# Kernel optimization log

Hardware: AMD Instinct MI355X
Metric: run time of the kernel (lower is better)

## Reference

```python
import jax, jax.numpy as jnp
import numpy as np

H = 4          # num_heads
MB = 4         # ttt mini_batch_size
GRP = 4        # scan_checkpoint_group_size
TTT_LR = 0.1   # ttt_base_lr
ERF_C = 0.7071067811865476   # 1/sqrt(2)
PDF_C = 0.3989422804014327   # 1/sqrt(2*pi)


def _gelu(z):
    return 0.5 * z * (1.0 + jax.scipy.special.erf(z * ERF_C))


def _gelu_grad(z):
    return 0.5 * (1.0 + jax.scipy.special.erf(z * ERF_C)) + z * jnp.exp(-0.5 * z * z) * PDF_C


def _ln(x, w, b, eps):
    mu = x.mean(-1, keepdims=True)
    var = ((x - mu) ** 2).mean(-1, keepdims=True)
    return w * (x - mu) / jnp.sqrt(var + eps) + b


def _ln_l2_bwd(z, w, b, target, eps=1e-6):
    # grad of 0.5*||LN(z; w, b) - target||^2 w.r.t. z (fused LN backward)
    mu = z.mean(-1, keepdims=True)
    var = ((z - mu) ** 2).mean(-1, keepdims=True)
    std = jnp.sqrt(var + eps)
    zhat = (z - mu) / std
    y = w * zhat + b
    g = w * (y - target)
    return (g - g.mean(-1, keepdims=True) - zhat * (g * zhat).mean(-1, keepdims=True)) / std


def _conv1d(x, w, b, pad):
    # x: [B, Cin, L], w: [Cout, Cin, K]
    y = jax.lax.conv_general_dilated(x, w, (1,), [(pad, pad)], dimension_numbers=("NCH", "OIH", "NCH"))
    return y + b[None, :, None]


def _ttt(x, wq, wk, wv, wo, W1, b1, W2, b2, lnw, lnb):
    # x: [B, L, D];  ttt_mlp fast-weight scan over mini-batches of size MB
    B, L, D = x.shape
    d = D // H
    nmb = L // MB
    ng = nmb // GRP

    def split(w):
        # [B,L,D] -> [ng, GRP, B, H, MB, d]
        return (x @ w).reshape(B, L, H, d).transpose(0, 2, 1, 3).reshape(B, H, ng, GRP, MB, d).transpose(2, 3, 0, 1, 4, 5)

    XQ, XK, XV = split(wq), split(wk), split(wv)
    lw = lnw[None, :, None, :]  # [1,H,1,d]
    lb = lnb[None, :, None, :]
    eta = TTT_LR / MB

    carry = (jnp.broadcast_to(W1, (B, H, d, 4 * d)),
             jnp.broadcast_to(b1, (B, H, 1, 4 * d)),
             jnp.broadcast_to(W2, (B, H, 4 * d, d)),
             jnp.broadcast_to(b2, (B, H, 1, d)))

    def step(c, inp):
        W1c, b1c, W2c, b2c = c
        xq, xk, xv = inp  # each [B,H,MB,d]
        Z1 = jnp.einsum('bhmd,bhdk->bhmk', xk, W1c) + b1c
        X2 = _gelu(Z1)
        Z2 = jnp.einsum('bhmk,bhkd->bhmd', X2, W2c) + b2c
        gZ2 = _ln_l2_bwd(Z2, lw, lb, xv - xk)
        gZ1 = jnp.einsum('bhmd,bhkd->bhmk', gZ2, W2c) * _gelu_grad(Z1)
        W1n = W1c - eta * jnp.einsum('bhmd,bhmk->bhdk', xk, gZ1)
        b1n = b1c - eta * gZ1.sum(2, keepdims=True)
        W2n = W2c - eta * jnp.einsum('bhmk,bhmd->bhkd', X2, gZ2)
        b2n = b2c - eta * gZ2.sum(2, keepdims=True)
        Z1q = jnp.einsum('bhmd,bhdk->bhmk', xq, W1n) + b1n
        Z2q = jnp.einsum('bhmk,bhkd->bhmd', _gelu(Z1q), W2n) + b2n
        return (W1n, b1n, W2n, b2n), xq + _ln(Z2q, lw, lb, 1e-6)

    @jax.checkpoint
    def group(c, inp_g):
        return jax.lax.scan(step, c, inp_g)

    _, out = jax.lax.scan(group, carry, (XQ, XK, XV))  # [ng,GRP,B,H,MB,d]
    out = out.transpose(2, 3, 0, 1, 4, 5).reshape(B, H, L, d).transpose(0, 2, 1, 3).reshape(B, L, D)
    return x + out @ wo


def reference(x, conv1_w, conv1_b, convs_w, convs_b, ln_w, ln_b, wq, wk, wv, wo,
              ttt_W1, ttt_b1, ttt_W2, ttt_b2, ttt_ln_w, ttt_ln_b,
              fc_w, fc_b, fc2_w, fc2_b, fc3_w, fc3_b):
    h = x.transpose(0, 2, 1)                       # [B, dim1, L]
    h = jax.nn.relu(_conv1d(h, conv1_w, conv1_b, 0))
    acts = []
    for i in range(8):
        h = jax.nn.relu(_conv1d(h, convs_w[i], convs_b[i], 1))
        acts.append(h)
    h = acts[1] + acts[3] + acts[5] + acts[7]      # x2 + x4 + x6 + x8
    h = h.transpose(0, 2, 1)                       # [B, L, dim3]
    h = _ln(h, ln_w, ln_b, 1e-5)
    h = _ttt(h, wq, wk, wv, wo, ttt_W1, ttt_b1, ttt_W2, ttt_b2, ttt_ln_w, ttt_ln_b)
    h = _ln(h, ln_w, ln_b, 1e-5)                   # module reuses self.layer_norm
    h = h @ fc_w + fc_b
    h = h @ fc2_w + fc2_b
    return h @ fc3_w + fc3_b                       # [B, L, 1]


def setup_inputs() -> dict:
    key = jax.random.key(0)
    ks = jax.random.split(key, 12)
    B, L, dim1, dim2, dim3 = 4, 1024, 64, 512, 256
    Hn, dh = 4, 64

    def n(k, shape):
        return jax.random.normal(k, shape, jnp.float32) * 0.02

    return {
        "x": jax.random.normal(ks[0], (B, L, dim1), jnp.float32),
        "conv1_w": n(ks[1], (dim3, dim1, 1)),
        "conv1_b": jnp.zeros((dim3,), jnp.float32),
        "convs_w": n(ks[2], (8, dim3, dim3, 3)),
        "convs_b": jnp.zeros((8, dim3), jnp.float32),
        "ln_w": jnp.ones((dim3,), jnp.float32),
        "ln_b": jnp.zeros((dim3,), jnp.float32),
        "wq": n(ks[3], (dim3, dim3)),
        "wk": n(ks[4], (dim3, dim3)),
        "wv": n(ks[5], (dim3, dim3)),
        "wo": n(ks[6], (dim3, dim3)),
        "ttt_W1": n(ks[7], (Hn, dh, 4 * dh)),
        "ttt_b1": jnp.zeros((Hn, 1, 4 * dh), jnp.float32),
        "ttt_W2": n(ks[8], (Hn, 4 * dh, dh)),
        "ttt_b2": jnp.zeros((Hn, 1, dh), jnp.float32),
        "ttt_ln_w": jnp.ones((Hn, dh), jnp.float32),
        "ttt_ln_b": jnp.zeros((Hn, dh), jnp.float32),
        "fc_w": n(ks[9], (dim3, dim2)),
        "fc_b": jnp.zeros((dim2,), jnp.float32),
        "fc2_w": n(ks[10], (dim2, dim1)),
        "fc2_b": jnp.zeros((dim1,), jnp.float32),
        "fc3_w": n(ks[11], (dim1, 1)),
        "fc3_b": jnp.zeros((1,), jnp.float32),
    }
```

## Files before the change

kernel.cpp:

```cpp
#include <hip/hip_runtime.h>
#include <hip/hip_bf16.h>


#define ERF_CF 0.70710678118654752f
#define PDF_CF 0.3989422804014327f
#define ETA 0.025f

typedef __attribute__((ext_vector_type(8))) short bfrag;
typedef __attribute__((ext_vector_type(4))) float f32x4;

union FB { bfrag v; unsigned short u[8]; unsigned d[4]; };

__device__ __forceinline__ float wsum(float v) {
#pragma unroll
  for (int o = 32; o > 0; o >>= 1) v += __shfl_xor(v, o, 64);
  return v;
}

__device__ __forceinline__ unsigned pack_split(float x) {
  unsigned u = __float_as_uint(x);
  unsigned hb = u & 0xFFFF0000u;
  float lf = x - __uint_as_float(hb);
  return hb | (__float_as_uint(lf) >> 16);
}
__device__ __forceinline__ float uns(unsigned short hs, unsigned short ls) {
  return __uint_as_float((unsigned)hs << 16) + __uint_as_float((unsigned)ls << 16);
}
__device__ __forceinline__ float fb_el(const FB& H, const FB& L, int e) {
  return __uint_as_float((unsigned)H.u[e] << 16) +
         __uint_as_float((unsigned)L.u[e] << 16);
}
__device__ __forceinline__ void split2(float f, unsigned short& hs, unsigned short& ls) {
  unsigned u = __float_as_uint(f);
  unsigned hb = u & 0xFFFF0000u;
  hs = (unsigned short)(u >> 16);
  ls = (unsigned short)(__float_as_uint(f - __uint_as_float(hb)) >> 16);
}
__device__ __forceinline__ f32x4 mm3(bfrag ah, bfrag al, bfrag bh, bfrag bl, f32x4 acc) {
  acc = __builtin_amdgcn_mfma_f32_16x16x32_bf16(ah, bh, acc, 0, 0, 0);
  acc = __builtin_amdgcn_mfma_f32_16x16x32_bf16(ah, bl, acc, 0, 0, 0);
  acc = __builtin_amdgcn_mfma_f32_16x16x32_bf16(al, bh, acc, 0, 0, 0);
  return acc;
}

__global__ void prep_w(const float* __restrict__ c1w, const float* __restrict__ cw,
                       float* __restrict__ wt1, float* __restrict__ wt) {
  int id = blockIdx.x * 256 + threadIdx.x;
  if (id < 16384) {
    int ci = id >> 8, co = id & 255;
    wt1[id] = c1w[co * 64 + ci];
  }
  int id2 = id - 16384;
  if (id2 >= 0 && id2 < 1572864) {
    int cv = id2 / 196608;
    int r = id2 - cv * 196608;
    int k = r >> 8, co = r & 255;
    int tt = k >> 8, ci = k & 255;
    wt[id2] = cw[((cv * 256 + co) * 256 + ci) * 3 + tt];
  }
}

__global__ void zero_halo(float* __restrict__ bufA, float* __restrict__ bufB) {
  int id = blockIdx.x * 256 + threadIdx.x;
  int c = id & 255;
  int row = (id >> 8) & 1;
  int b = (id >> 9) & 3;
  float* p = (id >> 11) ? bufB : bufA;
  p[(b * 1026 + row * 1025) * 256 + c] = 0.0f;
}

template <int BIAS, int RELU, int RES, int OST, int ACC>
__global__ __launch_bounds__(256) void gemm_k(
    const float* __restrict__ A, const float* __restrict__ Wt,
    const float* __restrict__ bias, const float* __restrict__ res,
    float* __restrict__ out, float* __restrict__ accp,
    int M, int N, int K, int lda, int haloA) {
  __shared__ float As[16][68];
  __shared__ float Bs[16][64];
  const int tid = threadIdx.x;
  const int bm = blockIdx.x * 64, bn = blockIdx.y * 64;
  const int tx = tid & 15, ty = tid >> 4;
  float acc[4][4] = {};

  for (int k0 = 0; k0 < K; k0 += 16) {
#pragma unroll
    for (int i = 0; i < 4; ++i) {
      int idx = tid + i * 256;
      int kk = idx & 15, mm = idx >> 4;
      int m = bm + mm;
      int rb = m * lda + (haloA ? ((m >> 10) << 9) : 0);
      As[kk][mm] = A[rb + k0 + kk];
    }
#pragma unroll
    for (int i = 0; i < 4; ++i) {
      int idx = tid + i * 256;
      int nn = idx & 63, kk = idx >> 6;
      Bs[kk][nn] = Wt[(k0 + kk) * N + bn + nn];
    }
    __syncthreads();
#pragma unroll
    for (int kk = 0; kk < 16; ++kk) {
      float4 av = *(const float4*)&As[kk][ty * 4];
      float4 bv = *(const float4*)&Bs[kk][tx * 4];
      float aa[4] = {av.x, av.y, av.z, av.w};
      float bb[4] = {bv.x, bv.y, bv.z, bv.w};
#pragma unroll
      for (int i = 0; i < 4; ++i)
#pragma unroll
        for (int j = 0; j < 4; ++j) acc[i][j] = fmaf(aa[i], bb[j], acc[i][j]);
    }
    __syncthreads();
  }

  const int n0 = bn + tx * 4;
#pragma unroll
  for (int i = 0; i < 4; ++i) {
    int m = bm + ty * 4 + i;
    int b_ = m >> 10, l = m & 1023;
    float v[4];
#pragma unroll
    for (int j = 0; j < 4; ++j) {
      float x = acc[i][j];
      if constexpr (BIAS) x += bias[n0 + j];
      if constexpr (RELU) x = fmaxf(x, 0.0f);
      if constexpr (RES) x += res[m * N + n0 + j];
      v[j] = x;
    }
    float4 vv = make_float4(v[0], v[1], v[2], v[3]);
    if constexpr (OST == 0) {
      *(float4*)&out[m * N + n0] = vv;
    } else if constexpr (OST == 1) {
      *(float4*)&out[(b_ * 1026 + l + 1) * 256 + n0] = vv;
    } else {
      int hq = n0 >> 6;
      int oidx = (((b_ * 4 + hq) * 1024 + l) << 6) + (n0 & 63);
      *(float4*)&out[oidx] = vv;
    }
    if constexpr (ACC == 1) {
      *(float4*)&accp[m * 256 + n0] = vv;
    } else if constexpr (ACC == 2) {
      float4 s = *(const float4*)&accp[m * 256 + n0];
      s.x += vv.x; s.y += vv.y; s.z += vv.z; s.w += vv.w;
      *(float4*)&accp[m * 256 + n0] = s;
    }
  }
}

__global__ __launch_bounds__(256) void ln_kernel(const float* __restrict__ in,
                                                 float* __restrict__ o,
                                                 const float* __restrict__ w,
                                                 const float* __restrict__ bb,
                                                 float eps) {
  int row = blockIdx.x * 4 + (threadIdx.x >> 6);
  int l = threadIdx.x & 63;
  float4 v = ((const float4*)(in + (long)row * 256))[l];
  float s = wsum(v.x + v.y + v.z + v.w);
  float mu = s * (1.0f / 256.0f);
  float dx = v.x - mu, dy = v.y - mu, dz = v.z - mu, dw = v.w - mu;
  float rstd = rsqrtf(wsum(dx * dx + dy * dy + dz * dz + dw * dw) * (1.0f / 256.0f) + eps);
  float4 wv = ((const float4*)w)[l];
  float4 bv = ((const float4*)bb)[l];
  float4 r;
  r.x = wv.x * dx * rstd + bv.x;
  r.y = wv.y * dy * rstd + bv.y;
  r.z = wv.z * dz * rstd + bv.z;
  r.w = wv.w * dw * rstd + bv.w;
  ((float4*)(o + (long)row * 256))[l] = r;
}

__global__ __launch_bounds__(512, 2) void ttt_mfma(
    const float* __restrict__ XQ, const float* __restrict__ XK,
    const float* __restrict__ XV, const float* __restrict__ W1i,
    const float* __restrict__ B1i, const float* __restrict__ W2i,
    const float* __restrict__ B2i, const float* __restrict__ LNW,
    const float* __restrict__ LNB, float* __restrict__ outp) {
  extern __shared__ char smem[];
  unsigned short* W2Hp  = (unsigned short*)smem;
  unsigned short* W2Lp  = W2Hp + 256 * 72;
  unsigned short* W2THp = W2Lp + 256 * 72;
  unsigned short* W2TLp = W2THp + 64 * 264;
  unsigned short* X2Hp  = W2TLp + 64 * 264;
  unsigned short* X2Lp  = X2Hp + 4 * 272;
  unsigned short* xkHp  = X2Lp + 4 * 272;
  unsigned short* xkLp  = xkHp + 4 * 80;
  unsigned short* xqHp  = xkLp + 4 * 80;
  unsigned short* xqLp  = xqHp + 4 * 80;
  unsigned short* gZHp  = xqLp + 4 * 80;
  unsigned short* gZLp  = gZHp + 4 * 80;
  float* X2F  = (float*)(gZLp + 4 * 80);
  float* gZ1f = X2F + 4 * 264;
  float* Z2f  = gZ1f + 1024;
  float* redS = Z2f + 256;
  float* xvL  = redS + 512;
  float* b2L  = xvL + 256;
  float* lwL  = b2L + 64;
  float* lbL  = lwL + 64;

  const int bh = blockIdx.x, b = bh >> 2, h = bh & 3;
  const int t = threadIdx.x;
  const int w8 = t >> 6;
  const int lane = t & 63;
  const int a = lane & 15, g = lane >> 4;
  const bool rowv = (a < 4), g0 = (g == 0);
  const int c0 = 32 * w8 + a;
  const int c1 = 32 * w8 + 16 + a;
  const int kh = w8 & 1;
  const int jc = (w8 >> 1) * 16 + a;

  FB zf; zf.d[0] = zf.d[1] = zf.d[2] = zf.d[3] = 0;

  FB w1h[2][2], w1l[2][2];
#pragma unroll
  for (int i = 0; i < 2; ++i) {
    int cc = 32 * w8 + i * 16 + a;
#pragma unroll
    for (int kc = 0; kc < 2; ++kc) {
#pragma unroll
      for (int e = 0; e < 8; ++e) {
        int k = kc * 32 + g * 8 + e;
        unsigned p = pack_split(W1i[(h * 64 + k) * 256 + cc]);
        w1h[i][kc].u[e] = (unsigned short)(p >> 16);
        w1l[i][kc].u[e] = (unsigned short)(p & 0xFFFFu);
      }
    }
  }
  float b1r0 = B1i[h * 256 + c0];
  float b1r1 = B1i[h * 256 + c1];

  for (int i = 0; i < 32; ++i) {
    int id = t + i * 512;
    int k = id >> 6, j = id & 63;
    unsigned p = pack_split(W2i[(h * 256 + k) * 64 + j]);
    W2Hp[k * 72 + j] = (unsigned short)(p >> 16);
    W2Lp[k * 72 + j] = (unsigned short)(p & 0xFFFFu);
    int j2 = id >> 8, k2 = id & 255;
    unsigned q = pack_split(W2i[(h * 256 + k2) * 64 + j2]);
    W2THp[j2 * 264 + k2] = (unsigned short)(q >> 16);
    W2TLp[j2 * 264 + k2] = (unsigned short)(q & 0xFFFFu);
  }
  if (t < 64) { b2L[t] = B2i[h * 64 + t]; lwL[t] = LNW[h * 64 + t]; lbL[t] = LNB[h * 64 + t]; }

  const long chain = (long)bh * 65536;
  float rk = 0.f, rv = 0.f, rq = 0.f;
  if (t >= 256) {
    int u = t - 256;
    rk = XK[chain + u]; rv = XV[chain + u]; rq = XQ[chain + u];
  }

  for (int n = 0; n < 256; ++n) {
    if (t >= 256) {
      int u = t - 256, m = u >> 6, k = u & 63;
      unsigned short hs, ls;
      split2(rk, hs, ls); xkHp[m * 80 + k] = hs; xkLp[m * 80 + k] = ls;
      split2(rq, hs, ls); xqHp[m * 80 + k] = hs; xqLp[m * 80 + k] = ls;
      xvL[u] = rv;
    }
    __syncthreads();

    float gpA[4] = {0.f, 0.f, 0.f, 0.f}, gpB[4] = {0.f, 0.f, 0.f, 0.f};

    {
      f32x4 A0 = (f32x4){b1r0, b1r0, b1r0, b1r0};
      f32x4 A1 = (f32x4){b1r1, b1r1, b1r1, b1r1};
#pragma unroll
      for (int kc = 0; kc < 2; ++kc) {
        int base = kc * 32 + g * 8;
        FB ah = zf, al = zf;
        if (rowv) {
          ah.v = *(const bfrag*)&xkHp[a * 80 + base];
          al.v = *(const bfrag*)&xkLp[a * 80 + base];
        }
        A0 = mm3(ah.v, al.v, w1h[0][kc].v, w1l[0][kc].v, A0);
        A1 = mm3(ah.v, al.v, w1h[1][kc].v, w1l[1][kc].v, A1);
      }
      if (g0) {
#pragma unroll
        for (int q = 0; q < 4; ++q) {
          float z = A0[q];
          float er = erff(z * ERF_CF);
          float hh = 0.5f * (1.0f + er);
          float x2 = z * hh;
          gpA[q] = hh + z * __expf(-0.5f * z * z) * PDF_CF;
          unsigned short hs, ls;
          split2(x2, hs, ls);
          X2Hp[q * 272 + c0] = hs; X2Lp[q * 272 + c0] = ls;
          X2F[q * 264 + c0] = x2;
          z = A1[q];
          er = erff(z * ERF_CF);
          hh = 0.5f * (1.0f + er);
          x2 = z * hh;
          gpB[q] = hh + z * __expf(-0.5f * z * z) * PDF_CF;
          split2(x2, hs, ls);
          X2Hp[q * 272 + c1] = hs; X2Lp[q * 272 + c1] = ls;
          X2F[q * 264 + c1] = x2;
        }
      }
    }
    __syncthreads();

    {
      f32x4 acc = (f32x4){0.f, 0.f, 0.f, 0.f};
#pragma unroll
      for (int k4 = 0; k4 < 4; ++k4) {
        int base = (kh * 4 + k4) * 32 + g * 8;
        FB ah = zf, al = zf, bhf, blf;
        if (rowv) {
          ah.v = *(const bfrag*)&X2Hp[a * 272 + base];
          al.v = *(const bfrag*)&X2Lp[a * 272 + base];
        }
        bhf.v = *(const bfrag*)&W2THp[jc * 264 + base];
        blf.v = *(const bfrag*)&W2TLp[jc * 264 + base];
        acc = mm3(ah.v, al.v, bhf.v, blf.v, acc);
      }
      if (g0) {
#pragma unroll
        for (int q = 0; q < 4; ++q) redS[(kh * 4 + q) * 64 + jc] = acc[q];
      }
    }
    __syncthreads();

    if (t < 256) {
      int m = w8, j = lane;
      float z2 = b2L[j] + redS[m * 64 + j] + redS[256 + m * 64 + j];
      float mu = wsum(z2) * (1.0f / 64.0f);
      float dv = z2 - mu;
      float var = wsum(dv * dv) * (1.0f / 64.0f);
      float stdv = sqrtf(var + 1e-6f);
      float zh = dv / stdv;
      float lw = lwL[j], lb = lbL[j];
      float xkf = uns(xkHp[m * 80 + j], xkLp[m * 80 + j]);
      float tgt = xvL[m * 64 + j] - xkf;
      float gg = lw * (lw * zh + lb - tgt);
      float gs = wsum(gg) * (1.0f / 64.0f);
      float gzs = wsum(gg * zh) * (1.0f / 64.0f);
      float gz2 = (gg - gs - zh * gzs) / stdv;
      unsigned short hs, ls;
      split2(gz2, hs, ls);
      gZHp[m * 80 + j] = hs; gZLp[m * 80 + j] = ls;
      Z2f[m * 64 + j] = gz2;
    } else if (n + 1 < 256) {
      int u = t - 256;
      long nb = chain + (long)(n + 1) * 256;
      rk = XK[nb + u]; rv = XV[nb + u]; rq = XQ[nb + u];
    }
    __syncthreads();

    {
      f32x4 A0 = (f32x4){0.f, 0.f, 0.f, 0.f};
      f32x4 A1 = (f32x4){0.f, 0.f, 0.f, 0.f};
#pragma unroll
      for (int kc = 0; kc < 2; ++kc) {
        int base = kc * 32 + g * 8;
        FB ah = zf, al = zf, b0h, b0l, b1h, b1l;
        if (rowv) {
          ah.v = *(const bfrag*)&gZHp[a * 80 + base];
          al.v = *(const bfrag*)&gZLp[a * 80 + base];
        }
        b0h.v = *(const bfrag*)&W2Hp[c0 * 72 + base];
        b0l.v = *(const bfrag*)&W2Lp[c0 * 72 + base];
        b1h.v = *(const bfrag*)&W2Hp[c1 * 72 + base];
        b1l.v = *(const bfrag*)&W2Lp[c1 * 72 + base];
        A0 = mm3(ah.v, al.v, b0h.v, b0l.v, A0);
        A1 = mm3(ah.v, al.v, b1h.v, b1l.v, A1);
      }
      if (g0) {
#pragma unroll
        for (int q = 0; q < 4; ++q) {
          gZ1f[q * 256 + c0] = A0[q] * gpA[q];
          gZ1f[q * 256 + c1] = A1[q] * gpB[q];
        }
      }
      {
        int jr = t & 63, kb = (t >> 6) * 32;
        float gz0 = Z2f[jr], gz1 = Z2f[64 + jr], gz2 = Z2f[128 + jr], gz3 = Z2f[192 + jr];
#pragma unroll
        for (int kk = 0; kk < 32; kk += 8) {
          int kb8 = kb + kk;
          float x0[8], x1[8], x2[8], x3[8];
          *(float4*)&x0[0] = *(const float4*)&X2F[kb8];        *(float4*)&x0[4] = *(const float4*)&X2F[kb8 + 4];
          *(float4*)&x1[0] = *(const float4*)&X2F[264 + kb8];  *(float4*)&x1[4] = *(const float4*)&X2F[264 + kb8 + 4];
          *(float4*)&x2[0] = *(const float4*)&X2F[528 + kb8];  *(float4*)&x2[4] = *(const float4*)&X2F[528 + kb8 + 4];
          *(float4*)&x3[0] = *(const float4*)&X2F[792 + kb8];  *(float4*)&x3[4] = *(const float4*)&X2F[792 + kb8 + 4];
          FB oh, ol, nh, nl;
          oh.v = *(const bfrag*)&W2THp[jr * 264 + kb8];
          ol.v = *(const bfrag*)&W2TLp[jr * 264 + kb8];
#pragma unroll
          for (int e = 0; e < 8; ++e) {
            float u = fmaf(x3[e], gz3, fmaf(x2[e], gz2, fmaf(x1[e], gz1, x0[e] * gz0)));
            float f = fmaf(-ETA, u, fb_el(oh, ol, e));
            unsigned short hs, ls;
            split2(f, hs, ls);
            nh.u[e] = hs; nl.u[e] = ls;
          }
          *(bfrag*)&W2THp[jr * 264 + kb8] = nh.v;
          *(bfrag*)&W2TLp[jr * 264 + kb8] = nl.v;
        }
      }
    }
    __syncthreads();

    {
      float gzA0 = gZ1f[c0], gzA1 = gZ1f[256 + c0], gzA2 = gZ1f[512 + c0], gzA3 = gZ1f[768 + c0];
      float gzB0 = gZ1f[c1], gzB1 = gZ1f[256 + c1], gzB2 = gZ1f[512 + c1], gzB3 = gZ1f[768 + c1];
      b1r0 = fmaf(-ETA, ((gzA0 + gzA1) + gzA2) + gzA3, b1r0);
      b1r1 = fmaf(-ETA, ((gzB0 + gzB1) + gzB2) + gzB3, b1r1);
#pragma unroll
      for (int kc = 0; kc < 2; ++kc) {
        int base = kc * 32 + g * 8;
        FB x0h, x0l, x1h, x1l, x2h, x2l, x3h, x3l;
        x0h.v = *(const bfrag*)&xkHp[base];       x0l.v = *(const bfrag*)&xkLp[base];
        x1h.v = *(const bfrag*)&xkHp[80 + base];  x1l.v = *(const bfrag*)&xkLp[80 + base];
        x2h.v = *(const bfrag*)&xkHp[160 + base]; x2l.v = *(const bfrag*)&xkLp[160 + base];
        x3h.v = *(const bfrag*)&xkHp[240 + base]; x3l.v = *(const bfrag*)&xkLp[240 + base];
#pragma unroll
        for (int e = 0; e < 8; ++e) {
          float k0 = fb_el(x0h, x0l, e), k1 = fb_el(x1h, x1l, e);
          float k2 = fb_el(x2h, x2l, e), k3 = fb_el(x3h, x3l, e);
          float uA = fmaf(k3, gzA3, fmaf(k2, gzA2, fmaf(k1, gzA1, k0 * gzA0)));
          float uB = fmaf(k3, gzB3, fmaf(k2, gzB2, fmaf(k1, gzB1, k0 * gzB0)));
          float fA = fmaf(-ETA, uA, fb_el(w1h[0][kc], w1l[0][kc], e));
          float fB = fmaf(-ETA, uB, fb_el(w1h[1][kc], w1l[1][kc], e));
          unsigned short hs, ls;
          split2(fA, hs, ls); w1h[0][kc].u[e] = hs; w1l[0][kc].u[e] = ls;
          split2(fB, hs, ls); w1h[1][kc].u[e] = hs; w1l[1][kc].u[e] = ls;
        }
      }
      {
        f32x4 A0 = (f32x4){b1r0, b1r0, b1r0, b1r0};
        f32x4 A1 = (f32x4){b1r1, b1r1, b1r1, b1r1};
#pragma unroll
        for (int kc = 0; kc < 2; ++kc) {
          int base = kc * 32 + g * 8;
          FB ah = zf, al = zf;
          if (rowv) {
            ah.v = *(const bfrag*)&xqHp[a * 80 + base];
            al.v = *(const bfrag*)&xqLp[a * 80 + base];
          }
          A0 = mm3(ah.v, al.v, w1h[0][kc].v, w1l[0][kc].v, A0);
          A1 = mm3(ah.v, al.v, w1h[1][kc].v, w1l[1][kc].v, A1);
        }
        if (g0) {
#pragma unroll
          for (int q = 0; q < 4; ++q) {
            float z = A0[q];
            float x2 = 0.5f * z * (1.0f + erff(z * ERF_CF));
            unsigned short hs, ls;
            split2(x2, hs, ls);
            X2Hp[q * 272 + c0] = hs; X2Lp[q * 272 + c0] = ls;
            z = A1[q];
            x2 = 0.5f * z * (1.0f + erff(z * ERF_CF));
            split2(x2, hs, ls);
            X2Hp[q * 272 + c1] = hs; X2Lp[q * 272 + c1] = ls;
          }
        }
      }
      {
        int kr = t & 255, jh = (t >> 8) * 32;
        float xk0 = X2F[kr], xk1 = X2F[264 + kr], xk2 = X2F[528 + kr], xk3 = X2F[792 + kr];
#pragma unroll
        for (int jj = 0; jj < 32; jj += 8) {
          int jb = jh + jj;
          float g0f[8], g1f[8], g2f[8], g3f[8];
          *(float4*)&g0f[0] = *(const float4*)&Z2f[jb];        *(float4*)&g0f[4] = *(const float4*)&Z2f[jb + 4];
          *(float4*)&g1f[0] = *(const float4*)&Z2f[64 + jb];   *(float4*)&g1f[4] = *(const float4*)&Z2f[64 + jb + 4];
          *(float4*)&g2f[0] = *(const float4*)&Z2f[128 + jb];  *(float4*)&g2f[4] = *(const float4*)&Z2f[128 + jb + 4];
          *(float4*)&g3f[0] = *(const float4*)&Z2f[192 + jb];  *(float4*)&g3f[4] = *(const float4*)&Z2f[192 + jb + 4];
          FB oh, ol, nh, nl;
          oh.v = *(const bfrag*)&W2Hp[kr * 72 + jb];
          ol.v = *(const bfrag*)&W2Lp[kr * 72 + jb];
#pragma unroll
          for (int e = 0; e < 8; ++e) {
            float u = fmaf(xk3, g3f[e], fmaf(xk2, g2f[e], fmaf(xk1, g1f[e], xk0 * g0f[e])));
            float f = fmaf(-ETA, u, fb_el(oh, ol, e));
            unsigned short hs, ls;
            split2(f, hs, ls);
            nh.u[e] = hs; nl.u[e] = ls;
          }
          *(bfrag*)&W2Hp[kr * 72 + jb] = nh.v;
          *(bfrag*)&W2Lp[kr * 72 + jb] = nl.v;
        }
      }
      if (t < 64)
        b2L[t] -= ETA * (((Z2f[t] + Z2f[64 + t]) + Z2f[128 + t]) + Z2f[192 + t]);
    }
    __syncthreads();

    {
      f32x4 acc = (f32x4){0.f, 0.f, 0.f, 0.f};
#pragma unroll
      for (int k4 = 0; k4 < 4; ++k4) {
        int base = (kh * 4 + k4) * 32 + g * 8;
        FB ah = zf, al = zf, bhf, blf;
        if (rowv) {
          ah.v = *(const bfrag*)&X2Hp[a * 272 + base];
          al.v = *(const bfrag*)&X2Lp[a * 272 + base];
        }
        bhf.v = *(const bfrag*)&W2THp[jc * 264 + base];
        blf.v = *(const bfrag*)&W2TLp[jc * 264 + base];
        acc = mm3(ah.v, al.v, bhf.v, blf.v, acc);
      }
      if (g0) {
#pragma unroll
        for (int q = 0; q < 4; ++q) redS[(kh * 4 + q) * 64 + jc] = acc[q];
      }
    }
    __syncthreads();

    if (t < 256) {
      int m = w8, j = lane;
      float z = b2L[j] + redS[m * 64 + j] + redS[256 + m * 64 + j];
      float mu = wsum(z) * (1.0f / 64.0f);
      float dv = z - mu;
      float var = wsum(dv * dv) * (1.0f / 64.0f);
      float rstd = rsqrtf(var + 1e-6f);
      float xqf = uns(xqHp[m * 80 + j], xqLp[m * 80 + j]);
      float val = lwL[j] * dv * rstd + lbL[j] + xqf;
      outp[((long)(b * 1024 + n * 4 + m)) * 256 + h * 64 + j] = val;
    }
    __syncthreads();
  }
}

__global__ __launch_bounds__(256) void fc3_kernel(const float* __restrict__ f2,
                                                  const float* __restrict__ w,
                                                  const float* __restrict__ bias,
                                                  float* __restrict__ o) {
  int m = blockIdx.x * 4 + (threadIdx.x >> 6);
  int lane = threadIdx.x & 63;
  float v = f2[m * 64 + lane] * w[lane];
  v = wsum(v);
  if (lane == 0) o[m] = v + bias[0];
}

extern "C" void kernel_launch(void* const* d_in, const int* in_sizes, int n_in,
                              void* d_out, int out_size, void* d_ws, size_t ws_size,
                              hipStream_t stream) {
  const float* x       = (const float*)d_in[0];
  const float* conv1_w = (const float*)d_in[1];
  const float* conv1_b = (const float*)d_in[2];
  const float* convs_w = (const float*)d_in[3];
  const float* convs_b = (const float*)d_in[4];
  const float* ln_w    = (const float*)d_in[5];
  const float* ln_b    = (const float*)d_in[6];
  const float* wq      = (const float*)d_in[7];
  const float* wk      = (const float*)d_in[8];
  const float* wv      = (const float*)d_in[9];
  const float* wo      = (const float*)d_in[10];
  const float* ttt_W1  = (const float*)d_in[11];
  const float* ttt_b1  = (const float*)d_in[12];
  const float* ttt_W2  = (const float*)d_in[13];
  const float* ttt_b2  = (const float*)d_in[14];
  const float* ttt_lnw = (const float*)d_in[15];
  const float* ttt_lnb = (const float*)d_in[16];
  const float* fc_w    = (const float*)d_in[17];
  const float* fc_b    = (const float*)d_in[18];
  const float* fc2_w   = (const float*)d_in[19];
  const float* fc2_b   = (const float*)d_in[20];
  const float* fc3_w   = (const float*)d_in[21];
  const float* fc3_b   = (const float*)d_in[22];

  float* ws = (float*)d_ws;
  float* wt1  = ws + 0;
  float* wt   = ws + 16384;
  float* bufA = ws + 1589248;
  float* bufB = ws + 2639872;
  float* sum4 = ws + 3690496;
  float* tln  = ws + 4739072;
  float* XQ   = ws + 5787648;
  float* XK   = ws + 6836224;
  float* XV   = ws + 7884800;
  float* tout = ws + 8933376;
  float* tfull = sum4;
  float* h2    = bufA;
  float* f1    = XQ;
  float* f2    = tout;

  const int M = 4096;
  dim3 blk(256);

  zero_halo<<<16, blk, 0, stream>>>(bufA, bufB);
  prep_w<<<6208, blk, 0, stream>>>(conv1_w, convs_w, wt1, wt);

  gemm_k<1, 1, 0, 1, 0><<<dim3(64, 4), blk, 0, stream>>>(
      x, wt1, conv1_b, nullptr, bufA, nullptr, M, 256, 64, 64, 0);

  for (int i = 0; i < 8; ++i) {
    const float* in = (i % 2 == 0) ? bufA : bufB;
    float* out = (i % 2 == 0) ? bufB : bufA;
    const float* wp = wt + (size_t)i * 196608;
    const float* bp = convs_b + i * 256;
    if (i == 1)
      gemm_k<1, 1, 0, 1, 1><<<dim3(64, 4), blk, 0, stream>>>(
          in, wp, bp, nullptr, out, sum4, M, 256, 768, 256, 1);
    else if (i == 3 || i == 5 || i == 7)
      gemm_k<1, 1, 0, 1, 2><<<dim3(64, 4), blk, 0, stream>>>(
          in, wp, bp, nullptr, out, sum4, M, 256, 768, 256, 1);
    else
      gemm_k<1, 1, 0, 1, 0><<<dim3(64, 4), blk, 0, stream>>>(
          in, wp, bp, nullptr, out, sum4, M, 256, 768, 256, 1);
  }

  ln_kernel<<<1024, blk, 0, stream>>>(sum4, tln, ln_w, ln_b, 1e-5f);

  gemm_k<0, 0, 0, 2, 0><<<dim3(64, 4), blk, 0, stream>>>(
      tln, wq, nullptr, nullptr, XQ, nullptr, M, 256, 256, 256, 0);
  gemm_k<0, 0, 0, 2, 0><<<dim3(64, 4), blk, 0, stream>>>(
      tln, wk, nullptr, nullptr, XK, nullptr, M, 256, 256, 256, 0);
  gemm_k<0, 0, 0, 2, 0><<<dim3(64, 4), blk, 0, stream>>>(
      tln, wv, nullptr, nullptr, XV, nullptr, M, 256, 256, 256, 0);

  const int TTT_LDS = 162688;
  (void)hipFuncSetAttribute((const void*)ttt_mfma,
                            hipFuncAttributeMaxDynamicSharedMemorySize, TTT_LDS);
  ttt_mfma<<<16, dim3(512), TTT_LDS, stream>>>(XQ, XK, XV, ttt_W1, ttt_b1,
                                               ttt_W2, ttt_b2, ttt_lnw, ttt_lnb,
                                               tout);

  gemm_k<0, 0, 1, 0, 0><<<dim3(64, 4), blk, 0, stream>>>(
      tout, wo, nullptr, tln, tfull, nullptr, M, 256, 256, 256, 0);

  ln_kernel<<<1024, blk, 0, stream>>>(tfull, h2, ln_w, ln_b, 1e-5f);

  gemm_k<1, 0, 0, 0, 0><<<dim3(64, 8), blk, 0, stream>>>(
      h2, fc_w, fc_b, nullptr, f1, nullptr, M, 512, 256, 256, 0);
  gemm_k<1, 0, 0, 0, 0><<<dim3(64, 1), blk, 0, stream>>>(
      f1, fc2_w, fc2_b, nullptr, f2, nullptr, M, 64, 512, 512, 0);
  fc3_kernel<<<1024, blk, 0, stream>>>(f2, fc3_w, fc3_b, (float*)d_out);
}
```

Before: 3.056 ms.

## Split TTT scan block into two 512-thread warp groups with specialized roles

Doubles the TTT kernel block to 1024 threads. The first 512 threads keep the W1-side work (Z1, GELU, gZ1, W1/b1 updates). The second 512 handle the W2-side GEMMs, the W2/W2T weight updates and the input prefetch, so the two weight updates can proceed concurrently within a phase. It also prefetches W2T fragments into registers during the Z1 phase. In exchange, per-thread register budget is halved and each barrier now covers 16 waves, with idle threads in some phases.

```diff
diff --git a/kernel.cpp b/kernel.cpp
--- a/kernel.cpp
+++ b/kernel.cpp
@@ -168,7 +168,7 @@
   ((float4*)(o + (long)row * 256))[l] = r;
 }
 
-__global__ __launch_bounds__(512, 2) void ttt_mfma(
+__global__ __launch_bounds__(1024, 4) void ttt_mfma(
     const float* __restrict__ XQ, const float* __restrict__ XK,
     const float* __restrict__ XV, const float* __restrict__ W1i,
     const float* __restrict__ B1i, const float* __restrict__ W2i,
@@ -198,37 +198,48 @@
 
   const int bh = blockIdx.x, b = bh >> 2, h = bh & 3;
   const int t = threadIdx.x;
-  const int w8 = t >> 6;
+  const bool isA = t < 512;
   const int lane = t & 63;
   const int a = lane & 15, g = lane >> 4;
   const bool rowv = (a < 4), g0 = (g == 0);
-  const int c0 = 32 * w8 + a;
-  const int c1 = 32 * w8 + 16 + a;
-  const int kh = w8 & 1;
-  const int jc = (w8 >> 1) * 16 + a;
+  const int wA = t >> 6;
+  const int c0 = isA ? (32 * wA + a) : 0;
+  const int c1 = isA ? (32 * wA + 16 + a) : 16;
+  const int u = t - 512;
+  const int wB = (t >> 6) & 7;
+  const int kh = wB & 1;
+  const int jc = (wB >> 1) * 16 + a;
 
   FB zf; zf.d[0] = zf.d[1] = zf.d[2] = zf.d[3] = 0;
 
   FB w1h[2][2], w1l[2][2];
-#pragma unroll
-  for (int i = 0; i < 2; ++i) {
-    int cc = 32 * w8 + i * 16 + a;
-#pragma unroll
-    for (int kc = 0; kc < 2; ++kc) {
-#pragma unroll
-      for (int e = 0; e < 8; ++e) {
-        int k = kc * 32 + g * 8 + e;
-        unsigned p = pack_split(W1i[(h * 64 + k) * 256 + cc]);
-        w1h[i][kc].u[e] = (unsigned short)(p >> 16);
-        w1l[i][kc].u[e] = (unsigned short)(p & 0xFFFFu);
-      }
-    }
-  }
-  float b1r0 = B1i[h * 256 + c0];
-  float b1r1 = B1i[h * 256 + c1];
-
-  for (int i = 0; i < 32; ++i) {
-    int id = t + i * 512;
+  float b1r0 = 0.f, b1r1 = 0.f;
+  if (isA) {
+#pragma unroll
+    for (int i = 0; i < 2; ++i) {
+      int cc = 32 * wA + i * 16 + a;
+#pragma unroll
+      for (int kc = 0; kc < 2; ++kc) {
+#pragma unroll
+        for (int e = 0; e < 8; ++e) {
+          int k = kc * 32 + g * 8 + e;
+          unsigned p = pack_split(W1i[(h * 64 + k) * 256 + cc]);
+          w1h[i][kc].u[e] = (unsigned short)(p >> 16);
+          w1l[i][kc].u[e] = (unsigned short)(p & 0xFFFFu);
+        }
+      }
+    }
+    b1r0 = B1i[h * 256 + c0];
+    b1r1 = B1i[h * 256 + c1];
+  } else {
+#pragma unroll
+    for (int i = 0; i < 2; ++i)
+#pragma unroll
+      for (int kc = 0; kc < 2; ++kc) { w1h[i][kc] = zf; w1l[i][kc] = zf; }
+  }
+
+  for (int i = 0; i < 16; ++i) {
+    int id = t + i * 1024;
     int k = id >> 6, j = id & 63;
     unsigned p = pack_split(W2i[(h * 256 + k) * 64 + j]);
     W2Hp[k * 72 + j] = (unsigned short)(p >> 16);
@@ -242,24 +253,30 @@
 
   const long chain = (long)bh * 65536;
   float rk = 0.f, rv = 0.f, rq = 0.f;
-  if (t >= 256) {
-    int u = t - 256;
-    rk = XK[chain + u]; rv = XV[chain + u]; rq = XQ[chain + u];
+  if (!isA) {
+    if (u < 256) { rk = XK[chain + u]; rv = XV[chain + u]; }
+    else         { rq = XQ[chain + (u - 256)]; }
   }
 
   for (int n = 0; n < 256; ++n) {
-    if (t >= 256) {
-      int u = t - 256, m = u >> 6, k = u & 63;
-      unsigned short hs, ls;
-      split2(rk, hs, ls); xkHp[m * 80 + k] = hs; xkLp[m * 80 + k] = ls;
-      split2(rq, hs, ls); xqHp[m * 80 + k] = hs; xqLp[m * 80 + k] = ls;
-      xvL[u] = rv;
+    if (!isA) {
+      if (u < 256) {
+        int m = u >> 6, k = u & 63;
+        unsigned short hs, ls;
+        split2(rk, hs, ls); xkHp[m * 80 + k] = hs; xkLp[m * 80 + k] = ls;
+        xvL[u] = rv;
+      } else {
+        int m = (u - 256) >> 6, k = (u - 256) & 63;
+        unsigned short hs, ls;
+        split2(rq, hs, ls); xqHp[m * 80 + k] = hs; xqLp[m * 80 + k] = ls;
+      }
     }
     __syncthreads();
 
     float gpA[4] = {0.f, 0.f, 0.f, 0.f}, gpB[4] = {0.f, 0.f, 0.f, 0.f};
-
-    {
+    FB wtH[4], wtL[4];
+
+    if (isA) {
       f32x4 A0 = (f32x4){b1r0, b1r0, b1r0, b1r0};
       f32x4 A1 = (f32x4){b1r1, b1r1, b1r1, b1r1};
 #pragma unroll
@@ -295,22 +312,27 @@
           X2F[q * 264 + c1] = x2;
         }
       }
-    }
-    __syncthreads();
-
-    {
-      f32x4 acc = (f32x4){0.f, 0.f, 0.f, 0.f};
+    } else {
 #pragma unroll
       for (int k4 = 0; k4 < 4; ++k4) {
         int base = (kh * 4 + k4) * 32 + g * 8;
-        FB ah = zf, al = zf, bhf, blf;
+        wtH[k4].v = *(const bfrag*)&W2THp[jc * 264 + base];
+        wtL[k4].v = *(const bfrag*)&W2TLp[jc * 264 + base];
+      }
+    }
+    __syncthreads();
+
+    if (!isA) {
+      f32x4 acc = (f32x4){0.f, 0.f, 0.f, 0.f};
+#pragma unroll
+      for (int k4 = 0; k4 < 4; ++k4) {
+        int base = (kh * 4 + k4) * 32 + g * 8;
+        FB ah = zf, al = zf;
         if (rowv) {
           ah.v = *(const bfrag*)&X2Hp[a * 272 + base];
           al.v = *(const bfrag*)&X2Lp[a * 272 + base];
         }
-        bhf.v = *(const bfrag*)&W2THp[jc * 264 + base];
-        blf.v = *(const bfrag*)&W2TLp[jc * 264 + base];
-        acc = mm3(ah.v, al.v, bhf.v, blf.v, acc);
+        acc = mm3(ah.v, al.v, wtH[k4].v, wtL[k4].v, acc);
       }
       if (g0) {
 #pragma unroll
@@ -320,7 +342,7 @@
     __syncthreads();
 
     if (t < 256) {
-      int m = w8, j = lane;
+      int m = t >> 6, j = lane;
       float z2 = b2L[j] + redS[m * 64 + j] + redS[256 + m * 64 + j];
       float mu = wsum(z2) * (1.0f / 64.0f);
       float dv = z2 - mu;
@@ -338,14 +360,14 @@
       split2(gz2, hs, ls);
       gZHp[m * 80 + j] = hs; gZLp[m * 80 + j] = ls;
       Z2f[m * 64 + j] = gz2;
-    } else if (n + 1 < 256) {
-      int u = t - 256;
+    } else if (!isA && n + 1 < 256) {
       long nb = chain + (long)(n + 1) * 256;
-      rk = XK[nb + u]; rv = XV[nb + u]; rq = XQ[nb + u];
-    }
-    __syncthreads();
-
-    {
+      if (u < 256) { rk = XK[nb + u]; rv = XV[nb + u]; }
+      else         { rq = XQ[nb + (u - 256)]; }
+    }
+    __syncthreads();
+
+    if (isA) {
       f32x4 A0 = (f32x4){0.f, 0.f, 0.f, 0.f};
       f32x4 A1 = (f32x4){0.f, 0.f, 0.f, 0.f};
 #pragma unroll
@@ -370,36 +392,35 @@
           gZ1f[q * 256 + c1] = A1[q] * gpB[q];
         }
       }
-      {
-        int jr = t & 63, kb = (t >> 6) * 32;
-        float gz0 = Z2f[jr], gz1 = Z2f[64 + jr], gz2 = Z2f[128 + jr], gz3 = Z2f[192 + jr];
-#pragma unroll
-        for (int kk = 0; kk < 32; kk += 8) {
-          int kb8 = kb + kk;
-          float x0[8], x1[8], x2[8], x3[8];
-          *(float4*)&x0[0] = *(const float4*)&X2F[kb8];        *(float4*)&x0[4] = *(const float4*)&X2F[kb8 + 4];
-          *(float4*)&x1[0] = *(const float4*)&X2F[264 + kb8];  *(float4*)&x1[4] = *(const float4*)&X2F[264 + kb8 + 4];
-          *(float4*)&x2[0] = *(const float4*)&X2F[528 + kb8];  *(float4*)&x2[4] = *(const float4*)&X2F[528 + kb8 + 4];
-          *(float4*)&x3[0] = *(const float4*)&X2F[792 + kb8];  *(float4*)&x3[4] = *(const float4*)&X2F[792 + kb8 + 4];
-          FB oh, ol, nh, nl;
-          oh.v = *(const bfrag*)&W2THp[jr * 264 + kb8];
-          ol.v = *(const bfrag*)&W2TLp[jr * 264 + kb8];
-#pragma unroll
-          for (int e = 0; e < 8; ++e) {
-            float u = fmaf(x3[e], gz3, fmaf(x2[e], gz2, fmaf(x1[e], gz1, x0[e] * gz0)));
-            float f = fmaf(-ETA, u, fb_el(oh, ol, e));
-            unsigned short hs, ls;
-            split2(f, hs, ls);
-            nh.u[e] = hs; nl.u[e] = ls;
-          }
-          *(bfrag*)&W2THp[jr * 264 + kb8] = nh.v;
-          *(bfrag*)&W2TLp[jr * 264 + kb8] = nl.v;
-        }
-      }
-    }
-    __syncthreads();
-
-    {
+    } else {
+      int jr = u & 63, kb = (u >> 6) * 32;
+      float gz0 = Z2f[jr], gz1 = Z2f[64 + jr], gz2 = Z2f[128 + jr], gz3 = Z2f[192 + jr];
+#pragma unroll
+      for (int kk = 0; kk < 32; kk += 8) {
+        int kb8 = kb + kk;
+        float x0[8], x1[8], x2[8], x3[8];
+        *(float4*)&x0[0] = *(const float4*)&X2F[kb8];        *(float4*)&x0[4] = *(const float4*)&X2F[kb8 + 4];
+        *(float4*)&x1[0] = *(const float4*)&X2F[264 + kb8];  *(float4*)&x1[4] = *(const float4*)&X2F[264 + kb8 + 4];
+        *(float4*)&x2[0] = *(const float4*)&X2F[528 + kb8];  *(float4*)&x2[4] = *(const float4*)&X2F[528 + kb8 + 4];
+        *(float4*)&x3[0] = *(const float4*)&X2F[792 + kb8];  *(float4*)&x3[4] = *(const float4*)&X2F[792 + kb8 + 4];
+        FB oh, ol, nh, nl;
+        oh.v = *(const bfrag*)&W2THp[jr * 264 + kb8];
+        ol.v = *(const bfrag*)&W2TLp[jr * 264 + kb8];
+#pragma unroll
+        for (int e = 0; e < 8; ++e) {
+          float uu = fmaf(x3[e], gz3, fmaf(x2[e], gz2, fmaf(x1[e], gz1, x0[e] * gz0)));
+          float f = fmaf(-ETA, uu, fb_el(oh, ol, e));
+          unsigned short hs, ls;
+          split2(f, hs, ls);
+          nh.u[e] = hs; nl.u[e] = ls;
+        }
+        *(bfrag*)&W2THp[jr * 264 + kb8] = nh.v;
+        *(bfrag*)&W2TLp[jr * 264 + kb8] = nl.v;
+      }
+    }
+    __syncthreads();
+
+    if (isA) {
       float gzA0 = gZ1f[c0], gzA1 = gZ1f[256 + c0], gzA2 = gZ1f[512 + c0], gzA3 = gZ1f[768 + c0];
       float gzB0 = gZ1f[c1], gzB1 = gZ1f[256 + c1], gzB2 = gZ1f[512 + c1], gzB3 = gZ1f[768 + c1];
       b1r0 = fmaf(-ETA, ((gzA0 + gzA1) + gzA2) + gzA3, b1r0);
@@ -454,38 +475,37 @@
           }
         }
       }
-      {
-        int kr = t & 255, jh = (t >> 8) * 32;
-        float xk0 = X2F[kr], xk1 = X2F[264 + kr], xk2 = X2F[528 + kr], xk3 = X2F[792 + kr];
-#pragma unroll
-        for (int jj = 0; jj < 32; jj += 8) {
-          int jb = jh + jj;
-          float g0f[8], g1f[8], g2f[8], g3f[8];
-          *(float4*)&g0f[0] = *(const float4*)&Z2f[jb];        *(float4*)&g0f[4] = *(const float4*)&Z2f[jb + 4];
-          *(float4*)&g1f[0] = *(const float4*)&Z2f[64 + jb];   *(float4*)&g1f[4] = *(const float4*)&Z2f[64 + jb + 4];
-          *(float4*)&g2f[0] = *(const float4*)&Z2f[128 + jb];  *(float4*)&g2f[4] = *(const float4*)&Z2f[128 + jb + 4];
-          *(float4*)&g3f[0] = *(const float4*)&Z2f[192 + jb];  *(float4*)&g3f[4] = *(const float4*)&Z2f[192 + jb + 4];
-          FB oh, ol, nh, nl;
-          oh.v = *(const bfrag*)&W2Hp[kr * 72 + jb];
-          ol.v = *(const bfrag*)&W2Lp[kr * 72 + jb];
-#pragma unroll
-          for (int e = 0; e < 8; ++e) {
-            float u = fmaf(xk3, g3f[e], fmaf(xk2, g2f[e], fmaf(xk1, g1f[e], xk0 * g0f[e])));
-            float f = fmaf(-ETA, u, fb_el(oh, ol, e));
-            unsigned short hs, ls;
-            split2(f, hs, ls);
-            nh.u[e] = hs; nl.u[e] = ls;
-          }
-          *(bfrag*)&W2Hp[kr * 72 + jb] = nh.v;
-          *(bfrag*)&W2Lp[kr * 72 + jb] = nl.v;
-        }
-      }
-      if (t < 64)
-        b2L[t] -= ETA * (((Z2f[t] + Z2f[64 + t]) + Z2f[128 + t]) + Z2f[192 + t]);
-    }
-    __syncthreads();
-
-    {
+    } else {
+      int kr = u & 255, jh = (u >> 8) * 32;
+      float xk0 = X2F[kr], xk1 = X2F[264 + kr], xk2 = X2F[528 + kr], xk3 = X2F[792 + kr];
+#pragma unroll
+      for (int jj = 0; jj < 32; jj += 8) {
+        int jb = jh + jj;
+        float g0f[8], g1f[8], g2f[8], g3f[8];
+        *(float4*)&g0f[0] = *(const float4*)&Z2f[jb];        *(float4*)&g0f[4] = *(const float4*)&Z2f[jb + 4];
+        *(float4*)&g1f[0] = *(const float4*)&Z2f[64 + jb];   *(float4*)&g1f[4] = *(const float4*)&Z2f[64 + jb + 4];
+        *(float4*)&g2f[0] = *(const float4*)&Z2f[128 + jb];  *(float4*)&g2f[4] = *(const float4*)&Z2f[128 + jb + 4];
+        *(float4*)&g3f[0] = *(const float4*)&Z2f[192 + jb];  *(float4*)&g3f[4] = *(const float4*)&Z2f[192 + jb + 4];
+        FB oh, ol, nh, nl;
+        oh.v = *(const bfrag*)&W2Hp[kr * 72 + jb];
+        ol.v = *(const bfrag*)&W2Lp[kr * 72 + jb];
+#pragma unroll
+        for (int e = 0; e < 8; ++e) {
+          float uu = fmaf(xk3, g3f[e], fmaf(xk2, g2f[e], fmaf(xk1, g1f[e], xk0 * g0f[e])));
+          float f = fmaf(-ETA, uu, fb_el(oh, ol, e));
+          unsigned short hs, ls;
+          split2(f, hs, ls);
+          nh.u[e] = hs; nl.u[e] = ls;
+        }
+        *(bfrag*)&W2Hp[kr * 72 + jb] = nh.v;
+        *(bfrag*)&W2Lp[kr * 72 + jb] = nl.v;
+      }
+      if (u < 64)
+        b2L[u] -= ETA * (((Z2f[u] + Z2f[64 + u]) + Z2f[128 + u]) + Z2f[192 + u]);
+    }
+    __syncthreads();
+
+    if (!isA) {
       f32x4 acc = (f32x4){0.f, 0.f, 0.f, 0.f};
 #pragma unroll
       for (int k4 = 0; k4 < 4; ++k4) {
@@ -507,7 +527,7 @@
     __syncthreads();
 
     if (t < 256) {
-      int m = w8, j = lane;
+      int m = t >> 6, j = lane;
       float z = b2L[j] + redS[m * 64 + j] + redS[256 + m * 64 + j];
       float mu = wsum(z) * (1.0f / 64.0f);
       float dv = z - mu;
@@ -612,9 +632,9 @@
   const int TTT_LDS = 162688;
   (void)hipFuncSetAttribute((const void*)ttt_mfma,
                             hipFuncAttributeMaxDynamicSharedMemorySize, TTT_LDS);
-  ttt_mfma<<<16, dim3(512), TTT_LDS, stream>>>(XQ, XK, XV, ttt_W1, ttt_b1,
-                                               ttt_W2, ttt_b2, ttt_lnw, ttt_lnb,
-                                               tout);
+  ttt_mfma<<<16, dim3(1024), TTT_LDS, stream>>>(XQ, XK, XV, ttt_W1, ttt_b1,
+                                                ttt_W2, ttt_b2, ttt_lnw, ttt_lnb,
+                                                tout);
 
   gemm_k<0, 0, 1, 0, 0><<<dim3(64, 4), blk, 0, stream>>>(
       tout, wo, nullptr, tln, tfull, nullptr, M, 256, 256, 256, 0);
```

After: 6.024 ms. 1.97x slower.
